# Kernel optimization log

Hardware: AMD Instinct MI355X
Metric: run time of the kernel (lower is better)

The kernel has to match this reference:

```python
import jax, jax.numpy as jnp
import numpy as np

D_MODEL = 1024
NUM_HEADS = 16
D_K = D_MODEL // NUM_HEADS


def setup_inputs() -> dict:
    key = jax.random.key(0)
    ks = jax.random.split(key, 11)
    B, S = 4, 2048
    s = 1.0 / np.sqrt(D_MODEL)
    inp = {
        "q": jax.random.normal(ks[0], (B, S, D_MODEL), jnp.float32),
        "k": jax.random.normal(ks[1], (B, S, D_MODEL), jnp.float32),
        "v": jax.random.normal(ks[2], (B, S, D_MODEL), jnp.float32),
        "w_q": jax.random.normal(ks[3], (D_MODEL, D_MODEL), jnp.float32) * s,
        "b_q": jnp.zeros((D_MODEL,), jnp.float32),
        "w_k": jax.random.normal(ks[4], (D_MODEL, D_MODEL), jnp.float32) * s,
        "b_k": jnp.zeros((D_MODEL,), jnp.float32),
        "w_v": jax.random.normal(ks[5], (D_MODEL, D_MODEL), jnp.float32) * s,
        "b_v": jnp.zeros((D_MODEL,), jnp.float32),
        "w_o": jax.random.normal(ks[6], (D_MODEL, D_MODEL), jnp.float32) * s,
        "b_o": jnp.zeros((D_MODEL,), jnp.float32),
    }
    return inp


def reference(q, k, v, w_q, b_q, w_k, b_k, w_v, b_v, w_o, b_o):
    B, S, _ = q.shape
    # projections; weights stored as [in, out] so x @ W + b
    def proj(x, w, b):
        y = x @ w + b  # [B, S, d_model]
        return y.reshape(B, -1, NUM_HEADS, D_K).transpose(0, 2, 1, 3)  # [B,H,S,d_k]
    qh = proj(q, w_q, b_q)
    kh = proj(k, w_k, b_k)
    vh = proj(v, w_v, b_v)
    scores = jnp.einsum("bhsd,bhtd->bhst", qh, kh) / jnp.sqrt(jnp.float32(D_K))
    attn = jax.nn.softmax(scores, axis=-1)  # dropout p=0.0 -> identity
    x = jnp.einsum("bhst,bhtd->bhsd", attn, vh)
    x = x.transpose(0, 2, 1, 3).reshape(B, S, D_MODEL)
    return x @ w_o + b_o
```

## Files before the change

### kernel.cpp

```cpp
#include <hip/hip_runtime.h>
#include <hip/hip_bf16.h>
#include <stdint.h>

#define D_MODEL 1024
#define SEQ 2048
#define BATCH 4
#define NHEADS 16
#define ROWS (BATCH*SEQ)

#define QKSCALE 0.18033688011f
#define DEFER_THR 11.5f

typedef __attribute__((ext_vector_type(4))) float f32x4;
typedef __attribute__((ext_vector_type(8))) short short8;

#if __has_builtin(__builtin_amdgcn_exp2f)
#define EXP2(x) __builtin_amdgcn_exp2f(x)
#else
#define EXP2(x) exp2f(x)
#endif

__device__ __forceinline__ unsigned short f2bf(float f) {
    unsigned int x = __builtin_bit_cast(unsigned int, f);
    x += 0x7fffu + ((x >> 16) & 1u);
    return (unsigned short)(x >> 16);
}

__device__ __forceinline__ unsigned int cvtpk(float a, float b) {
    unsigned int r;
    asm("v_cvt_pk_bf16_f32 %0, %1, %2" : "=v"(r) : "v"(a), "v"(b));
    return r;
}

__global__ __launch_bounds__(256) void wtrans_kernel(const float* __restrict__ w,
                                                     unsigned short* __restrict__ wt) {
    __shared__ float tile[32][33];
    int tx = threadIdx.x & 31;
    int ty = threadIdx.x >> 5;
    int r0 = blockIdx.y * 32, c0 = blockIdx.x * 32;
    #pragma unroll
    for (int i = 0; i < 4; ++i)
        tile[ty + 8*i][tx] = w[(size_t)(r0 + ty + 8*i) * D_MODEL + (c0 + tx)];
    __syncthreads();
    #pragma unroll
    for (int i = 0; i < 4; ++i) {
        int n = c0 + ty + 8*i;
        int k = r0 + tx;
        unsigned short val = f2bf(tile[tx][ty + 8*i]);
        size_t tidx = (size_t)(n >> 7) * 16 + (k >> 6);
        int row = n & 127;
        int byte = (row*128 + (k & 63)*2) ^ ((row & 7) << 4);
        *(unsigned short*)((char*)wt + tidx*16384 + byte) = val;
    }
}

template<int AF32, int OUTMODE, int QSCALE>
__global__ __launch_bounds__(256) void gemm_kernel(const void* __restrict__ Aptr,
                                                   const unsigned short* __restrict__ Bt,
                                                   const float* __restrict__ bias,
                                                   void* __restrict__ Out) {
    __shared__ __attribute__((aligned(16))) unsigned short Alds[128*64];
    __shared__ __attribute__((aligned(16))) unsigned short Blds[128*64];
    const int m0 = blockIdx.x * 128;
    const int n0 = blockIdx.y * 128;
    const int t = threadIdx.x;
    const int lane = t & 63;
    const int w = t >> 6;
    const int wm = w >> 1, wn = w & 1;
    const int l15 = lane & 15, lg = lane >> 4;

    f32x4 acc[4][4];
    #pragma unroll
    for (int i = 0; i < 4; ++i)
        #pragma unroll
        for (int j = 0; j < 4; ++j) acc[i][j] = (f32x4)(0.0f);

    for (int k0 = 0; k0 < D_MODEL; k0 += 64) {
        if (AF32) {
            const float* Af = (const float*)Aptr;
            #pragma unroll
            for (int i = 0; i < 8; ++i) {
                int idx = t + i*256;
                int row = idx >> 4, c4 = idx & 15;
                f32x4 v = *(const f32x4*)(Af + (size_t)(m0+row)*D_MODEL + k0 + c4*4);
                unsigned int lo = cvtpk(v[0], v[1]);
                unsigned int hi = cvtpk(v[2], v[3]);
                unsigned long long pk = (unsigned long long)lo
                                      | ((unsigned long long)hi << 32);
                int byte = (row*128 + c4*8) ^ ((row & 7) << 4);
                *(unsigned long long*)((char*)Alds + byte) = pk;
            }
        } else {
            const unsigned short* Ab = (const unsigned short*)Aptr;
            #pragma unroll
            for (int i = 0; i < 4; ++i) {
                int idx = t + i*256;
                int row = idx >> 3, c8 = idx & 7;
                short8 v = *(const short8*)(Ab + (size_t)(m0+row)*D_MODEL + k0 + c8*8);
                int byte = (row*128 + c8*16) ^ ((row & 7) << 4);
                *(short8*)((char*)Alds + byte) = v;
            }
        }
        {
            const unsigned short* tsrc = Bt + ((size_t)(n0 >> 7) * 16 + (k0 >> 6)) * 8192;
            const unsigned short* srcw = tsrc + (size_t)(w*4)*512 + lane*8;
            unsigned short* dstw = Blds + (w*4)*512;
            #pragma unroll
            for (int i = 0; i < 4; ++i) {
                __builtin_amdgcn_global_load_lds(
                    (const __attribute__((address_space(1))) void*)(srcw + i*512),
                    (__attribute__((address_space(3))) void*)(dstw + i*512),
                    16, 0, 0);
            }
        }
        __syncthreads();

        #pragma unroll
        for (int kk = 0; kk < 2; ++kk) {
            short8 af[4], bfr[4];
            #pragma unroll
            for (int mi = 0; mi < 4; ++mi) {
                int row = wm*64 + mi*16 + l15;
                int byte = (row*128 + kk*64 + lg*16) ^ ((row & 7) << 4);
                af[mi] = *(const short8*)((const char*)Alds + byte);
            }
            #pragma unroll
            for (int ni = 0; ni < 4; ++ni) {
                int row = wn*64 + ni*16 + l15;
                int byte = (row*128 + kk*64 + lg*16) ^ ((row & 7) << 4);
                bfr[ni] = *(const short8*)((const char*)Blds + byte);
            }
            #pragma unroll
            for (int mi = 0; mi < 4; ++mi)
                #pragma unroll
                for (int ni = 0; ni < 4; ++ni)
                    acc[mi][ni] = __builtin_amdgcn_mfma_f32_16x16x32_bf16(
                        af[mi], bfr[ni], acc[mi][ni], 0, 0, 0);
        }
        __syncthreads();
    }

    #pragma unroll
    for (int mi = 0; mi < 4; ++mi)
        #pragma unroll
        for (int ni = 0; ni < 4; ++ni) {
            int col = n0 + wn*64 + ni*16 + l15;
            float bv = bias[col];
            if (OUTMODE == 2) {
                int h = col >> 6, d = col & 63;
                int row0 = m0 + wm*64 + mi*16 + lg*4;
                int bb = row0 >> 11, s = row0 & 2047;
                unsigned long long pk = 0;
                #pragma unroll
                for (int r = 0; r < 4; ++r) {
                    float v = acc[mi][ni][r] + bv;
                    pk |= (unsigned long long)f2bf(v) << (16*r);
                }
                *(unsigned long long*)((unsigned short*)Out
                    + ((size_t)((bb*NHEADS + h)*64 + d))*SEQ + s) = pk;
            } else {
                #pragma unroll
                for (int r = 0; r < 4; ++r) {
                    int row = m0 + wm*64 + mi*16 + lg*4 + r;
                    float v = acc[mi][ni][r] + bv;
                    if (QSCALE) v *= QKSCALE;
                    if (OUTMODE == 1) {
                        int bb = row >> 11, s = row & 2047;
                        int h = col >> 6, d = col & 63;
                        ((unsigned short*)Out)[(((size_t)(bb*NHEADS + h)*SEQ + s) << 6) + d] = f2bf(v);
                    } else {
                        ((float*)Out)[(size_t)row*D_MODEL + col] = v;
                    }
                }
            }
        }
}

__global__ __launch_bounds__(256, 4) void attn_kernel(const unsigned short* __restrict__ qh,
                                                      const unsigned short* __restrict__ kh,
                                                      const unsigned short* __restrict__ vt,
                                                      unsigned short* __restrict__ xout) {
    __shared__ __attribute__((aligned(16))) unsigned short Klds[2][64*64];
    __shared__ __attribute__((aligned(16))) unsigned short Vtl[2][64*64];

    const int qb = blockIdx.x;
    const int bh = blockIdx.y;
    const int t = threadIdx.x;
    const int lane = t & 63;
    const int w = t >> 6;
    const int l15 = lane & 15, lg = lane >> 4;

    const unsigned short* qbase = qh + (size_t)bh * SEQ * 64;
    const unsigned short* kbase = kh + (size_t)bh * SEQ * 64;
    const unsigned short* vtbase = vt + (size_t)bh * 64 * SEQ;

    short8 qf[2][2];
    #pragma unroll
    for (int l = 0; l < 2; ++l) {
        int qrow = qb*128 + w*32 + l*16 + l15;
        qf[l][0] = *(const short8*)(qbase + (size_t)qrow*64 + lg*8);
        qf[l][1] = *(const short8*)(qbase + (size_t)qrow*64 + 32 + lg*8);
    }

    const int c8 = t & 7;
    const int r0 = t >> 3;
    const int r1 = r0 + 32;
    const int p0 = (r0 & 0x23) | ((r0 & 4) << 2) | ((r0 & 0x18) >> 1);
    const int p1 = (r1 & 0x23) | ((r1 & 4) << 2) | ((r1 & 0x18) >> 1);
    const int kb0 = (p0*128 + c8*16) ^ ((p0 & 7) << 4);
    const int kb1 = (p1*128 + c8*16) ^ ((p1 & 7) << 4);
    const int vb0 = (r0*128 + c8*16) ^ ((r0 & 7) << 4);
    const int vb1 = (r1*128 + c8*16) ^ ((r1 & 7) << 4);
    const unsigned short* kg0 = kbase + r0*64 + c8*8;
    const unsigned short* kg1 = kbase + r1*64 + c8*8;
    const unsigned short* vg0 = vtbase + (size_t)r0*SEQ + c8*8;
    const unsigned short* vg1 = vtbase + (size_t)r1*SEQ + c8*8;

    int fb[4][2];
    #pragma unroll
    for (int nb = 0; nb < 4; ++nb) {
        int rr = nb*16 + l15;
        int sw = (rr & 7) << 4;
        fb[nb][0] = (rr*128 + lg*16) ^ sw;
        fb[nb][1] = (rr*128 + 64 + lg*16) ^ sw;
    }

    float m[2] = {-1e30f, -1e30f}, lsum[2] = {0.f, 0.f};
    f32x4 o[2][4];
    #pragma unroll
    for (int l = 0; l < 2; ++l)
        #pragma unroll
        for (int nb = 0; nb < 4; ++nb) o[l][nb] = (f32x4)(0.0f);

    short8 kr0 = *(const short8*)(kg0);
    short8 kr1 = *(const short8*)(kg1);
    short8 vr0 = *(const short8*)(vg0);
    short8 vr1 = *(const short8*)(vg1);
    *(short8*)((char*)Klds[0] + kb0) = kr0;
    *(short8*)((char*)Klds[0] + kb1) = kr1;
    *(short8*)((char*)Vtl[0] + vb0) = vr0;
    *(short8*)((char*)Vtl[0] + vb1) = vr1;
    __syncthreads();

    const int NT = SEQ/64;
    #pragma unroll 2
    for (int ti = 0; ti < NT; ++ti) {
        const int c = ti & 1;
        if (ti + 1 < NT) {
            int off = (ti + 1) * 64;
            kr0 = *(const short8*)(kg0 + (size_t)off*64);
            kr1 = *(const short8*)(kg1 + (size_t)off*64);
            vr0 = *(const short8*)(vg0 + off);
            vr1 = *(const short8*)(vg1 + off);
        }
        const char* Kc = (const char*)Klds[c];
        const char* Vc = (const char*)Vtl[c];

        f32x4 s4[2][4];
        #pragma unroll
        for (int nb = 0; nb < 4; ++nb) {
            short8 kf0 = *(const short8*)(Kc + fb[nb][0]);
            short8 kf1 = *(const short8*)(Kc + fb[nb][1]);
            #pragma unroll
            for (int l = 0; l < 2; ++l) {
                f32x4 s = (f32x4)(0.0f);
                s = __builtin_amdgcn_mfma_f32_16x16x32_bf16(kf0, qf[l][0], s, 0, 0, 0);
                s = __builtin_amdgcn_mfma_f32_16x16x32_bf16(kf1, qf[l][1], s, 0, 0, 0);
                s4[l][nb] = s;
            }
        }

        union U { short8 s; unsigned int u[4]; } pa[2][2];
        #pragma unroll
        for (int l = 0; l < 2; ++l) {
            float tm = s4[l][0][0];
            #pragma unroll
            for (int nb = 0; nb < 4; ++nb)
                #pragma unroll
                for (int r = 0; r < 4; ++r) tm = fmaxf(tm, s4[l][nb][r]);
            tm = fmaxf(tm, __shfl_xor(tm, 16));
            tm = fmaxf(tm, __shfl_xor(tm, 32));

            if (__any(tm > m[l] + DEFER_THR)) {
                float mnew = fmaxf(m[l], tm);
                float alpha = EXP2(m[l] - mnew);
                lsum[l] *= alpha;
                m[l] = mnew;
                #pragma unroll
                for (int r = 0; r < 4; ++r) {
                    float ar = __shfl(alpha, lg*4 + r);
                    #pragma unroll
                    for (int nb = 0; nb < 4; ++nb) o[l][nb][r] *= ar;
                }
            }

            float p[16];
            float ts = 0.f;
            #pragma unroll
            for (int nb = 0; nb < 4; ++nb)
                #pragma unroll
                for (int r = 0; r < 4; ++r) {
                    float pv = EXP2(s4[l][nb][r] - m[l]);
                    p[nb*4 + r] = pv;
                    ts += pv;
                }
            ts += __shfl_xor(ts, 16);
            ts += __shfl_xor(ts, 32);
            lsum[l] += ts;

            pa[l][0].u[0] = cvtpk(p[0],  p[1]);  pa[l][0].u[1] = cvtpk(p[2],  p[3]);
            pa[l][0].u[2] = cvtpk(p[4],  p[5]);  pa[l][0].u[3] = cvtpk(p[6],  p[7]);
            pa[l][1].u[0] = cvtpk(p[8],  p[9]);  pa[l][1].u[1] = cvtpk(p[10], p[11]);
            pa[l][1].u[2] = cvtpk(p[12], p[13]); pa[l][1].u[3] = cvtpk(p[14], p[15]);
        }

        #pragma unroll
        for (int nb = 0; nb < 4; ++nb) {
            short8 vf0 = *(const short8*)(Vc + fb[nb][0]);
            short8 vf1 = *(const short8*)(Vc + fb[nb][1]);
            o[0][nb] = __builtin_amdgcn_mfma_f32_16x16x32_bf16(pa[0][0].s, vf0, o[0][nb], 0, 0, 0);
            o[0][nb] = __builtin_amdgcn_mfma_f32_16x16x32_bf16(pa[0][1].s, vf1, o[0][nb], 0, 0, 0);
            o[1][nb] = __builtin_amdgcn_mfma_f32_16x16x32_bf16(pa[1][0].s, vf0, o[1][nb], 0, 0, 0);
            o[1][nb] = __builtin_amdgcn_mfma_f32_16x16x32_bf16(pa[1][1].s, vf1, o[1][nb], 0, 0, 0);
        }

        if (ti + 1 < NT) {
            *(short8*)((char*)Klds[c^1] + kb0) = kr0;
            *(short8*)((char*)Klds[c^1] + kb1) = kr1;
            *(short8*)((char*)Vtl[c^1] + vb0) = vr0;
            *(short8*)((char*)Vtl[c^1] + vb1) = vr1;
        }
        __syncthreads();
    }

    const int bb = bh >> 4, h = bh & 15;
    #pragma unroll
    for (int l = 0; l < 2; ++l) {
        float rl[4];
        #pragma unroll
        for (int r = 0; r < 4; ++r) rl[r] = 1.0f / __shfl(lsum[l], lg*4 + r);
        #pragma unroll
        for (int nb = 0; nb < 4; ++nb)
            #pragma unroll
            for (int r = 0; r < 4; ++r) {
                int s = qb*128 + w*32 + l*16 + lg*4 + r;
                int d = nb*16 + l15;
                xout[((size_t)(bb*SEQ + s))*D_MODEL + h*64 + d] = f2bf(o[l][nb][r] * rl[r]);
            }
    }
}

extern "C" void kernel_launch(void* const* d_in, const int* in_sizes, int n_in,
                              void* d_out, int out_size, void* d_ws, size_t ws_size,
                              hipStream_t stream) {
    (void)in_sizes; (void)n_in; (void)out_size; (void)ws_size;
    const float* q  = (const float*)d_in[0];
    const float* k  = (const float*)d_in[1];
    const float* v  = (const float*)d_in[2];
    const float* wq = (const float*)d_in[3];
    const float* bq = (const float*)d_in[4];
    const float* wk = (const float*)d_in[5];
    const float* bk = (const float*)d_in[6];
    const float* wv = (const float*)d_in[7];
    const float* bv = (const float*)d_in[8];
    const float* wo = (const float*)d_in[9];
    const float* bo = (const float*)d_in[10];

    char* ws = (char*)d_ws;
    unsigned short* wqt = (unsigned short*)(ws);
    unsigned short* wkt = (unsigned short*)(ws + (2ull << 20));
    unsigned short* wvt = (unsigned short*)(ws + (4ull << 20));
    unsigned short* wot = (unsigned short*)(ws + (6ull << 20));
    unsigned short* qhd = (unsigned short*)(ws + (8ull << 20));
    unsigned short* khd = (unsigned short*)(ws + (24ull << 20));
    unsigned short* vtd = (unsigned short*)(ws + (40ull << 20));
    unsigned short* xat = (unsigned short*)(ws + (56ull << 20));

    dim3 tgrid(D_MODEL/32, D_MODEL/32);
    hipLaunchKernelGGL(wtrans_kernel, tgrid, dim3(256), 0, stream, wq, wqt);
    hipLaunchKernelGGL(wtrans_kernel, tgrid, dim3(256), 0, stream, wk, wkt);
    hipLaunchKernelGGL(wtrans_kernel, tgrid, dim3(256), 0, stream, wv, wvt);
    hipLaunchKernelGGL(wtrans_kernel, tgrid, dim3(256), 0, stream, wo, wot);

    dim3 ggrid(ROWS/128, D_MODEL/128);
    hipLaunchKernelGGL((gemm_kernel<1,1,1>), ggrid, dim3(256), 0, stream,
                       (const void*)q, wqt, bq, (void*)qhd);
    hipLaunchKernelGGL((gemm_kernel<1,1,0>), ggrid, dim3(256), 0, stream,
                       (const void*)k, wkt, bk, (void*)khd);
    hipLaunchKernelGGL((gemm_kernel<1,2,0>), ggrid, dim3(256), 0, stream,
                       (const void*)v, wvt, bv, (void*)vtd);

    hipLaunchKernelGGL(attn_kernel, dim3(SEQ/128, BATCH*NHEADS), dim3(256), 0, stream,
                       qhd, khd, vtd, xat);

    hipLaunchKernelGGL((gemm_kernel<0,0,0>), ggrid, dim3(256), 0, stream,
                       (const void*)xat, wot, bo, d_out);
}
```

Measured before the change: 234.0 us.

## Vectorize weight transpose, add MFMA priority hints, defer softmax row-sum reduction

The weight transpose kernel now packs eight bf16 values per thread and issues 16-byte stores instead of scalar 2-byte stores. MFMA blocks in the GEMM and attention kernels are wrapped in s_setprio raises so waves issuing matrix ops get scheduling priority. In attention, exp2 is computed speculatively before the max check and recomputed only when a rescale triggers. The per-tile cross-lane sum shuffles move to a single reduction at the end. This trims shuffle and latency overhead per tile, but the transpose uses only half the threads and exp work is repeated on the rare rescale path.

```diff
diff --git a/kernel.cpp b/kernel.cpp
--- a/kernel.cpp
+++ b/kernel.cpp
@@ -13,6 +13,7 @@
 
 typedef __attribute__((ext_vector_type(4))) float f32x4;
 typedef __attribute__((ext_vector_type(8))) short short8;
+typedef __attribute__((ext_vector_type(4))) unsigned int uint4v;
 
 #if __has_builtin(__builtin_amdgcn_exp2f)
 #define EXP2(x) __builtin_amdgcn_exp2f(x)
@@ -42,15 +43,20 @@
     for (int i = 0; i < 4; ++i)
         tile[ty + 8*i][tx] = w[(size_t)(r0 + ty + 8*i) * D_MODEL + (c0 + tx)];
     __syncthreads();
-    #pragma unroll
-    for (int i = 0; i < 4; ++i) {
-        int n = c0 + ty + 8*i;
-        int k = r0 + tx;
-        unsigned short val = f2bf(tile[tx][ty + 8*i]);
-        size_t tidx = (size_t)(n >> 7) * 16 + (k >> 6);
+    int t = threadIdx.x;
+    if (t < 128) {
+        int n_loc = t >> 2;
+        int kc = t & 3;
+        int n = c0 + n_loc;
+        int kbase = r0 + kc*8;
+        uint4v pk;
+        #pragma unroll
+        for (int j = 0; j < 4; ++j)
+            pk[j] = cvtpk(tile[kc*8 + 2*j][n_loc], tile[kc*8 + 2*j + 1][n_loc]);
+        size_t tidx = (size_t)(n >> 7) * 16 + (kbase >> 6);
         int row = n & 127;
-        int byte = (row*128 + (k & 63)*2) ^ ((row & 7) << 4);
-        *(unsigned short*)((char*)wt + tidx*16384 + byte) = val;
+        int byte = (row*128 + (kbase & 63)*2) ^ ((row & 7) << 4);
+        *(uint4v*)((char*)wt + tidx*16384 + byte) = pk;
     }
 }
 
@@ -130,12 +136,14 @@
                 int byte = (row*128 + kk*64 + lg*16) ^ ((row & 7) << 4);
                 bfr[ni] = *(const short8*)((const char*)Blds + byte);
             }
+            __builtin_amdgcn_s_setprio(1);
             #pragma unroll
             for (int mi = 0; mi < 4; ++mi)
                 #pragma unroll
                 for (int ni = 0; ni < 4; ++ni)
                     acc[mi][ni] = __builtin_amdgcn_mfma_f32_16x16x32_bf16(
                         af[mi], bfr[ni], acc[mi][ni], 0, 0, 0);
+            __builtin_amdgcn_s_setprio(0);
         }
         __syncthreads();
     }
@@ -261,6 +269,7 @@
         for (int nb = 0; nb < 4; ++nb) {
             short8 kf0 = *(const short8*)(Kc + fb[nb][0]);
             short8 kf1 = *(const short8*)(Kc + fb[nb][1]);
+            __builtin_amdgcn_s_setprio(1);
             #pragma unroll
             for (int l = 0; l < 2; ++l) {
                 f32x4 s = (f32x4)(0.0f);
@@ -268,11 +277,23 @@
                 s = __builtin_amdgcn_mfma_f32_16x16x32_bf16(kf1, qf[l][1], s, 0, 0, 0);
                 s4[l][nb] = s;
             }
+            __builtin_amdgcn_s_setprio(0);
         }
 
         union U { short8 s; unsigned int u[4]; } pa[2][2];
         #pragma unroll
         for (int l = 0; l < 2; ++l) {
+            float p[16];
+            float ts = 0.f;
+            #pragma unroll
+            for (int nb = 0; nb < 4; ++nb)
+                #pragma unroll
+                for (int r = 0; r < 4; ++r) {
+                    float pv = EXP2(s4[l][nb][r] - m[l]);
+                    p[nb*4 + r] = pv;
+                    ts += pv;
+                }
+
             float tm = s4[l][0][0];
             #pragma unroll
             for (int nb = 0; nb < 4; ++nb)
@@ -292,20 +313,16 @@
                     #pragma unroll
                     for (int nb = 0; nb < 4; ++nb) o[l][nb][r] *= ar;
                 }
-            }
-
-            float p[16];
-            float ts = 0.f;
-            #pragma unroll
-            for (int nb = 0; nb < 4; ++nb)
-                #pragma unroll
-                for (int r = 0; r < 4; ++r) {
-                    float pv = EXP2(s4[l][nb][r] - m[l]);
-                    p[nb*4 + r] = pv;
-                    ts += pv;
-                }
-            ts += __shfl_xor(ts, 16);
-            ts += __shfl_xor(ts, 32);
+                ts = 0.f;
+                #pragma unroll
+                for (int nb = 0; nb < 4; ++nb)
+                    #pragma unroll
+                    for (int r = 0; r < 4; ++r) {
+                        float pv = EXP2(s4[l][nb][r] - m[l]);
+                        p[nb*4 + r] = pv;
+                        ts += pv;
+                    }
+            }
             lsum[l] += ts;
 
             pa[l][0].u[0] = cvtpk(p[0],  p[1]);  pa[l][0].u[1] = cvtpk(p[2],  p[3]);
@@ -318,10 +335,12 @@
         for (int nb = 0; nb < 4; ++nb) {
             short8 vf0 = *(const short8*)(Vc + fb[nb][0]);
             short8 vf1 = *(const short8*)(Vc + fb[nb][1]);
+            __builtin_amdgcn_s_setprio(1);
             o[0][nb] = __builtin_amdgcn_mfma_f32_16x16x32_bf16(pa[0][0].s, vf0, o[0][nb], 0, 0, 0);
             o[0][nb] = __builtin_amdgcn_mfma_f32_16x16x32_bf16(pa[0][1].s, vf1, o[0][nb], 0, 0, 0);
             o[1][nb] = __builtin_amdgcn_mfma_f32_16x16x32_bf16(pa[1][0].s, vf0, o[1][nb], 0, 0, 0);
             o[1][nb] = __builtin_amdgcn_mfma_f32_16x16x32_bf16(pa[1][1].s, vf1, o[1][nb], 0, 0, 0);
+            __builtin_amdgcn_s_setprio(0);
         }
 
         if (ti + 1 < NT) {
@@ -336,9 +355,12 @@
     const int bb = bh >> 4, h = bh & 15;
     #pragma unroll
     for (int l = 0; l < 2; ++l) {
+        float lt = lsum[l];
+        lt += __shfl_xor(lt, 16);
+        lt += __shfl_xor(lt, 32);
         float rl[4];
         #pragma unroll
-        for (int r = 0; r < 4; ++r) rl[r] = 1.0f / __shfl(lsum[l], lg*4 + r);
+        for (int r = 0; r < 4; ++r) rl[r] = 1.0f / __shfl(lt, lg*4 + r);
         #pragma unroll
         for (int nb = 0; nb < 4; ++nb)
             #pragma unroll
```

Result: slower. 263.3 us (+12.5%).
